# Optimization experiments

Hardware: AMD Instinct MI355X
Metric: run time of the kernel (lower is better)

## Reference

```python
import jax, jax.numpy as jnp
import numpy as np

B, L1, L2, D1, D2, H, P = 32, 256, 64, 256, 256, 256, 128
I = D1 + D2  # gate / GRU input dim


def setup_inputs() -> dict:
    key = jax.random.key(0)
    ks = jax.random.split(key, 10)
    s = 0.05  # weight init scale
    return {
        "sequence1": jax.random.normal(ks[0], (B, L1, D1), jnp.float32),
        "sequence2": jax.random.normal(ks[1], (B, L2, D2), jnp.float32),
        "sequence1_mask": jnp.ones((B, L1), jnp.float32),
        "sequence2_mask": jnp.ones((B, L2), jnp.float32),
        "W1": jax.random.normal(ks[2], (D2, P), jnp.float32) * s,
        "W2": jax.random.normal(ks[3], (D1 + H, P), jnp.float32) * s,
        "v": jax.random.normal(ks[4], (P,), jnp.float32) * s,
        "Wg": jax.random.normal(ks[5], (I, I), jnp.float32) * s,
        "bg": jnp.zeros((I,), jnp.float32),
        "w_ih": jax.random.normal(ks[6], (3 * H, I), jnp.float32) * s,
        "w_hh": jax.random.normal(ks[7], (3 * H, H), jnp.float32) * s,
        "b_ih": jnp.zeros((3 * H,), jnp.float32),
        "b_hh": jnp.zeros((3 * H,), jnp.float32),
    }


def reference(sequence1, sequence2, sequence1_mask, sequence2_mask,
              W1, W2, v, Wg, bg, w_ih, w_hh, b_ih, b_hh):
    # Precompute sequence2 projection once: [B, L2, P]
    seq2_proj = jnp.einsum('bld,dp->blp', sequence2, W1)
    # Additive mask for softmax over L2
    neg = jnp.where(sequence2_mask > 0, 0.0, -1e9)  # [B, L2]
    xs = jnp.transpose(sequence1, (1, 0, 2))  # [L1, B, D1]

    def step(h, x_t):
        # attention: v^T tanh(W1*seq2_j + W2*[x_t; h])
        vec = jnp.concatenate([x_t, h], axis=-1)            # [B, D1+H]
        s = jnp.einsum('blp,p->bl',
                       jnp.tanh(seq2_proj + (vec @ W2)[:, None, :]), v) + neg
        w = jax.nn.softmax(s, axis=-1)                      # [B, L2]
        att = jnp.einsum('bl,bld->bd', w, sequence2)        # [B, D2]
        inp = jnp.concatenate([x_t, att], axis=-1)          # [B, I]
        # gated attention: sigmoid(Linear(inp)) * inp
        inp = jax.nn.sigmoid(inp @ Wg.T + bg) * inp
        # GRUCell (torch semantics)
        gi = inp @ w_ih.T + b_ih
        gh = h @ w_hh.T + b_hh
        ir, iz, inn = jnp.split(gi, 3, axis=-1)
        hr, hz, hn = jnp.split(gh, 3, axis=-1)
        r = jax.nn.sigmoid(ir + hr)
        z = jax.nn.sigmoid(iz + hz)
        n = jnp.tanh(inn + r * hn)
        h_new = (1.0 - z) * n + z * h
        return h_new, h_new

    h0 = jnp.zeros((sequence1.shape[0], w_hh.shape[1]), sequence1.dtype)
    _, hs = jax.lax.scan(step, h0, xs)                      # [L1, B, H]
    out = jnp.transpose(hs, (1, 0, 2)) * sequence1_mask[:, :, None]
    return out
```

## Files before the change

### kernel.cpp

```cpp
#include <hip/hip_runtime.h>

typedef _Float16 half2_v __attribute__((ext_vector_type(2)));
typedef unsigned int u32;

#define W2K_O    0
#define WHHP_O   16384
#define WIHP_O   114688
#define NPACKW   311296
#define S2P_B    1245184
#define S2T_B    1769472
#define M1_B     2818048
#define PROJX_B  4915200
#define GATEX_B  7012352
#define EXCH_B   15400960

#define SMEM_BYTES 149520

__device__ __forceinline__ float fdot2(half2_v a, half2_v b, float c) {
    return __builtin_amdgcn_fdot2(a, b, c, false);
}
__device__ __forceinline__ half2_v h2_of(u32 u) { return __builtin_bit_cast(half2_v, u); }
__device__ __forceinline__ u32 pack_h2(float a, float b) {
    half2_v r; r[0] = (_Float16)a; r[1] = (_Float16)b;
    return __builtin_bit_cast(u32, r);
}
__device__ __forceinline__ float dot4(uint4 w, uint4 a, float acc) {
    acc = fdot2(h2_of(w.x), h2_of(a.x), acc);
    acc = fdot2(h2_of(w.y), h2_of(a.y), acc);
    acc = fdot2(h2_of(w.z), h2_of(a.z), acc);
    acc = fdot2(h2_of(w.w), h2_of(a.w), acc);
    return acc;
}
__device__ __forceinline__ float fast_tanh(float x) {
    float e = __expf(2.0f * x);
    return 1.0f - 2.0f / (e + 1.0f);
}
__device__ __forceinline__ float fast_sigmoid(float x) {
    return 1.0f / (1.0f + __expf(-x));
}
__device__ __forceinline__ u32 aload(const u32* p) {
    return __hip_atomic_load(p, __ATOMIC_RELAXED, __HIP_MEMORY_SCOPE_AGENT);
}
__device__ __forceinline__ void astore(u32* p, u32 v) {
    __hip_atomic_store(p, v, __ATOMIC_RELAXED, __HIP_MEMORY_SCOPE_AGENT);
}
__device__ __forceinline__ u32 mkw(float x, u32 st) {
    unsigned short hb = __builtin_bit_cast(unsigned short, (_Float16)x);
    return (st << 16) | (u32)hb;
}
__device__ __forceinline__ float f16low(u32 v) {
    return (float)__builtin_bit_cast(_Float16, (unsigned short)(v & 0xFFFFu));
}

__global__ void prep_pack_w(const float* __restrict__ W2, const float* __restrict__ wih,
                            const float* __restrict__ whh, u32* __restrict__ ws_u) {
    int idx = blockIdx.x * 256 + threadIdx.x;
    if (idx >= NPACKW) return;
    float a, c;
    if (idx < WHHP_O) {
        int mm = idx >> 11, r = idx & 2047, p = r >> 4, kl = r & 15;
        int row = 256 + mm * 32 + 2 * kl;
        a = W2[row * 128 + p]; c = W2[(row + 1) * 128 + p];
    } else if (idx < WIHP_O) {
        int t2 = idx - WHHP_O, mm = t2 / 12288, r = t2 % 12288, o = r >> 7, k = r & 127;
        int row = (o >> 5) * 256 + mm * 32 + (o & 31);
        a = whh[row * 256 + 2 * k]; c = whh[row * 256 + 2 * k + 1];
    } else {
        int t2 = idx - WIHP_O, mm = t2 / 24576, r = t2 % 24576, o = r >> 8, k = r & 255;
        int row = (o >> 5) * 256 + mm * 32 + (o & 31);
        a = wih[row * 512 + 2 * k]; c = wih[row * 512 + 2 * k + 1];
    }
    ws_u[idx] = pack_h2(a, c);
}

__global__ void prep_s2p(const float* __restrict__ seq2, const float* __restrict__ W1,
                         _Float16* __restrict__ outh) {
    int idx = blockIdx.x * 256 + threadIdx.x;
    int p = idx & 127, j = (idx >> 7) & 63, b = idx >> 13;
    const float* s2 = seq2 + (b * 64 + j) * 256;
    float acc = 0.f;
    #pragma unroll 8
    for (int d = 0; d < 256; ++d) acc += s2[d] * W1[d * 128 + p];
    outh[idx] = (_Float16)acc;
}

__global__ void prep_s2T(const float* __restrict__ seq2, _Float16* __restrict__ dst) {
    int idx = blockIdx.x * 256 + threadIdx.x;
    int j = idx & 63, d = (idx >> 6) & 255, b = idx >> 14;
    dst[idx] = (_Float16)seq2[(b * 64 + j) * 256 + d];
}

__global__ void prep_m1(const float* __restrict__ Wg, const float* __restrict__ seq2,
                        _Float16* __restrict__ dst) {
    int idx = blockIdx.x * 256 + threadIdx.x;
    int j = idx & 63, o = (idx >> 6) & 511, b = idx >> 15;
    const float* wr = Wg + o * 512 + 256;
    const float* s2 = seq2 + (b * 64 + j) * 256;
    float acc = 0.f;
    #pragma unroll 8
    for (int d = 0; d < 256; ++d) acc += wr[d] * s2[d];
    dst[idx] = (_Float16)acc;
}

__global__ void prep_gemm(const float* __restrict__ A, const float* __restrict__ Bsrc,
                          int mode, _Float16* __restrict__ C, int N) {
    __shared__ float As[64][17];
    __shared__ float Bs[16][65];
    int r0 = blockIdx.x * 64, n0 = blockIdx.y * 64;
    int tid = threadIdx.x;
    int tr = tid >> 4, tc = tid & 15;
    float acc[4][4] = {};
    for (int k0 = 0; k0 < 256; k0 += 16) {
        #pragma unroll
        for (int i = 0; i < 4; ++i) {
            int rr = (tid >> 4) + i * 16, kk = tid & 15;
            As[rr][kk] = A[(r0 + rr) * 256 + k0 + kk];
        }
        #pragma unroll
        for (int i = 0; i < 4; ++i) {
            if (mode == 0) { int kk = (tid >> 6) + i * 4, nn = tid & 63; Bs[kk][nn] = Bsrc[(k0 + kk) * N + n0 + nn]; }
            else           { int nn = (tid >> 4) + i * 16, kk = tid & 15; Bs[kk][nn] = Bsrc[(n0 + nn) * 512 + k0 + kk]; }
        }
        __syncthreads();
        #pragma unroll
        for (int k = 0; k < 16; ++k)
            #pragma unroll
            for (int i = 0; i < 4; ++i)
                #pragma unroll
                for (int j = 0; j < 4; ++j)
                    acc[i][j] += As[tr * 4 + i][k] * Bs[k][tc * 4 + j];
        __syncthreads();
    }
    for (int i = 0; i < 4; ++i)
        for (int j = 0; j < 4; ++j)
            C[(size_t)(r0 + tr * 4 + i) * N + n0 + tc * 4 + j] = (_Float16)acc[i][j];
}

__global__ void __launch_bounds__(1024) match_rnn(
    const float* __restrict__ seq1, const float* __restrict__ mask1,
    const float* __restrict__ mask2, const float* __restrict__ v,
    const float* __restrict__ bg, const float* __restrict__ bih,
    const float* __restrict__ bhh, char* __restrict__ ws, float* __restrict__ out)
{
    const int m = blockIdx.x >> 5;
    const int b = blockIdx.x & 31;
    const int tid = threadIdx.x;

    extern __shared__ char smem[];
    u32* s_whh4 = (u32*)smem;
    u32* s_wih4 = s_whh4 + 12288;
    u32* s_w2k  = s_wih4 + 12288;
    u32* s_s2pU = s_w2k + 2176;
    u32* s_m1u  = s_s2pU + 4608;
    u32* s_s2Tu = s_m1u + 2112;
    float* s_redA = (float*)(s_s2Tu + 2112);
    float* s_redD = s_redA + 96;
    u32* s_h2u  = (u32*)(s_redD + 96);
    u32* s_ip2a = s_h2u + 160;
    u32* s_ip2b = s_ip2a + 160;
    float* s_projh = (float*)(s_ip2b + 160);
    float* s_projx = s_projh + 144;
    float* s_v   = s_projx + 144;
    float* s_w   = s_v + 144;
    float* s_neg = s_w + 64;
    float* s_gx  = s_neg + 64;
    float* s_xc  = s_gx + 64;
    float* s_bg  = s_xc + 64;
    float* s_bih = s_bg + 64;
    float* s_bhh = s_bih + 96;
    float* s_hf  = s_bhh + 96;
    u32* s_hloc  = (u32*)(s_hf + 32);
    float* s_m1v = (float*)(s_hloc + 16);

    unsigned short* s_s2p  = (unsigned short*)s_s2pU;
    unsigned short* s_h2h  = (unsigned short*)s_h2u;
    unsigned short* s_ip2ah = (unsigned short*)s_ip2a;
    unsigned short* s_ip2bh = (unsigned short*)s_ip2b;

    const u32* wsrc = (const u32*)ws;

    for (int i = tid; i < 12288; i += 1024) {
        int o = i >> 7, k = i & 127, u = k >> 2;
        int du4 = ((o >> 3) * 256) + ((u & 3) * 64) + (((o & 7) << 3) | (u >> 2));
        s_whh4[du4 * 4 + (k & 3)] = wsrc[WHHP_O + m * 12288 + i];
    }
    for (int i = tid; i < 12288; i += 1024) {
        int o = i >> 7, k = i & 127, u = k >> 2;
        int du4 = ((o >> 3) * 256) + ((u & 3) * 64) + (((o & 7) << 3) | (u >> 2));
        s_wih4[du4 * 4 + (k & 3)] = wsrc[WIHP_O + m * 24576 + o * 256 + k];
    }
    for (int i = tid; i < 2048; i += 1024) {
        int p = i >> 4, kl = i & 15;
        s_w2k[p * 17 + kl] = wsrc[W2K_O + m * 2048 + i];
    }
    {
        const u32* s2src = wsrc + (S2P_B / 4) + b * 4096;
        for (int i = tid; i < 4096; i += 1024) {
            int j = i >> 6, kk = i & 63;
            s_s2pU[j * 72 + kk] = s2src[i];
        }
        const u32* m1src = wsrc + (M1_B / 4) + (b * 512 + m * 64) * 32;
        for (int i = tid; i < 2048; i += 1024) {
            int o = i >> 5, jw = i & 31;
            s_m1u[o * 33 + jw] = m1src[i];
        }
        if (m >= 4) {
            const u32* stsrc = wsrc + (S2T_B / 4) + (b * 256 + (m - 4) * 64) * 32;
            for (int i = tid; i < 2048; i += 1024) {
                int dd = i >> 5, jw = i & 31;
                s_s2Tu[dd * 33 + jw] = stsrc[i];
            }
        } else {
            for (int i = tid; i < 2112; i += 1024) s_s2Tu[i] = 0u;
        }
    }
    if (tid < 128) s_v[tid + (tid >> 3)] = v[tid];
    if (tid < 64) { s_neg[tid] = (mask2[b * 64 + tid] > 0.f) ? 0.f : -1e9f; s_bg[tid] = bg[m * 64 + tid]; }
    if (tid < 96) {
        int row = (tid >> 5) * 256 + m * 32 + (tid & 31);
        s_bih[tid] = bih[row]; s_bhh[tid] = bhh[row];
    }
    if (tid < 32) s_hf[tid] = 0.f;

    uint4 wiA = {}, wiB = {}, wiC = {}, wiD = {};
    const int oAD = ((tid >> 6) << 3) + ((tid & 63) >> 3);
    const int ksAD = tid & 7;
    if (tid < 768) {
        const uint4* wip = (const uint4*)(wsrc + WIHP_O + m * 24576 + oAD * 256 + 128 + ksAD * 16);
        wiA = wip[0]; wiB = wip[1]; wiC = wip[2]; wiD = wip[3];
    }

    u32* exch = (u32*)(ws + EXCH_B) + b * 2048;
    const u32* g_projx = (const u32*)(ws + PROJX_B);
    const u32* g_gatex = (const u32*)(ws + GATEX_B);

    int dead = 0;
    __syncthreads();

    for (int t = 0; t < 256; ++t) {
        const u32 st = (u32)(t + 1);
        float4 xv = {};
        u32 pxv = 0, gxv = 0; float mkv = 0.f;
        if (tid >= 896 && tid < 912) {
            if (m < 4)
                xv = ((const float4*)(seq1 + (size_t)(b * 256 + t) * 256 + m * 64))[tid - 896];
        } else if (tid >= 912 && tid < 976)
            pxv = g_projx[(b * 256 + t) * 64 + (tid - 912)];
        else if (tid >= 976 && tid < 1008)
            gxv = g_gatex[(b * 256 + t) * 256 + m * 32 + (tid - 976)];
        else if (tid == 1008)
            mkv = mask1[b * 256 + t];

        if (t > 0) {
            u32 v1, v2;
            const bool p2 = tid < 256;
            const u32 stp = (u32)t;
            if (!dead) {
                int sp = 0;
                for (;;) {
                    v1 = aload(exch + tid);
                    v2 = p2 ? aload(exch + 1024 + tid) : (stp << 16);
                    bool ok = ((v1 >> 16) == stp) && ((v2 >> 16) == stp);
                    if (__all((int)ok)) break;
                    __builtin_amdgcn_s_sleep(1);
                    if (++sp > (1 << 17)) { dead = 1; break; }
                }
            } else { v1 = aload(exch + tid); v2 = p2 ? aload(exch + 1024 + tid) : 0; }
            float ph = f16low(v1);
            ph += __shfl_down(ph, 4, 8);
            ph += __shfl_down(ph, 2, 8);
            ph += __shfl_down(ph, 1, 8);
            if ((tid & 7) == 0) { int p = tid >> 3; s_projh[p + (p >> 3)] = ph; }
            if (p2) {
                int k = tid;
                int pos = ((k >> 5) * 20 + ((k >> 1) & 15)) * 2 + (k & 1);
                s_h2h[pos] = (unsigned short)(v2 & 0xFFFFu);
            }
        } else {
            if (tid < 160) s_h2u[tid] = 0u;
            if (tid < 144) s_projh[tid] = 0.f;
        }
        if (tid >= 896 && tid < 912) {
            int q = tid - 896;
            s_xc[4 * q] = xv.x; s_xc[4 * q + 1] = xv.y; s_xc[4 * q + 2] = xv.z; s_xc[4 * q + 3] = xv.w;
        } else if (tid >= 912 && tid < 976) {
            half2_v h = h2_of(pxv); int i = tid - 912;
            int base = 2 * i + (i >> 2);
            s_projx[base] = (float)h[0]; s_projx[base + 1] = (float)h[1];
        } else if (tid >= 976 && tid < 1008) {
            half2_v h = h2_of(gxv); int i = tid - 976;
            s_gx[2 * i] = (float)h[0]; s_gx[2 * i + 1] = (float)h[1];
        } else if (tid == 1008) s_m1v[0] = mkv;
        __syncthreads();

        {
            int j = tid >> 4, pk = tid & 15, p0 = pk * 8, pb = pk * 9;
            uint4 sv = *(const uint4*)&s_s2p[j * 144 + p0];
            const u32* su = (const u32*)&sv;
            float acc = 0.f;
            #pragma unroll
            for (int q = 0; q < 4; ++q) {
                half2_v h = h2_of(su[q]);
                int pc = pb + 2 * q;
                float a0 = (float)h[0] + s_projx[pc] + s_projh[pc];
                float a1 = (float)h[1] + s_projx[pc + 1] + s_projh[pc + 1];
                acc += fast_tanh(a0) * s_v[pc];
                acc += fast_tanh(a1) * s_v[pc + 1];
            }
            acc += __shfl_down(acc, 8, 16);
            acc += __shfl_down(acc, 4, 16);
            acc += __shfl_down(acc, 2, 16);
            acc += __shfl_down(acc, 1, 16);
            if (pk == 0) s_w[j] = acc + s_neg[j];
        }
        __syncthreads();
        if (tid < 64) {
            float sc = s_w[tid], mx = sc;
            #pragma unroll
            for (int off = 32; off > 0; off >>= 1) mx = fmaxf(mx, __shfl_xor(mx, off));
            float e = __expf(sc - mx), s = e;
            #pragma unroll
            for (int off = 32; off > 0; off >>= 1) s += __shfl_xor(s, off);
            s_w[tid] = e / s;
        }
        __syncthreads();

        if (tid < 512) {
            int o = tid >> 3, r = tid & 7, q = r & 3;
            const u32* src = (r >= 4) ? &s_s2Tu[o * 33] : &s_m1u[o * 33];
            float acc = 0.f;
            #pragma unroll
            for (int c = 0; c < 8; ++c) {
                half2_v h = h2_of(src[q * 8 + c]);
                int j0 = (q * 8 + c) * 2;
                acc += (float)h[0] * s_w[j0] + (float)h[1] * s_w[j0 + 1];
            }
            acc += __shfl_down(acc, 2, 4);
            acc += __shfl_down(acc, 1, 4);
            float attv = __shfl_down(acc, 4, 8);
            if (r == 0) {
                float g = acc + s_gx[o] + s_bg[o];
                float inpv = (m < 4) ? s_xc[o] : attv;
                astore(&exch[1280 + m * 64 + o], mkw(fast_sigmoid(g) * inpv, st));
            }
        }
        if (tid < 768) {
            const uint4* wbase = (const uint4*)s_whh4 + (tid >> 6) * 256;
            float acc = 0.f;
            #pragma unroll
            for (int c = 0; c < 4; ++c) {
                uint4 wv4 = wbase[c * 64 + (tid & 63)];
                uint4 av = *(const uint4*)&s_h2u[ksAD * 20 + c * 4];
                acc = dot4(wv4, av, acc);
            }
            acc += __shfl_down(acc, 4, 8);
            acc += __shfl_down(acc, 2, 8);
            acc += __shfl_down(acc, 1, 8);
            if (ksAD == 0) s_redA[oAD] = acc + s_bhh[oAD];
        }
        if (tid < 512) {
            u32 vv;
            if (!dead) {
                int sp = 0;
                for (;;) {
                    vv = aload(exch + 1280 + tid);
                    if (__all((int)((vv >> 16) == st))) break;
                    __builtin_amdgcn_s_sleep(1);
                    if (++sp > (1 << 17)) { dead = 1; break; }
                }
            } else vv = aload(exch + 1280 + tid);
            int i = tid;
            if (i < 256) {
                int pos = ((i >> 5) * 20 + ((i >> 1) & 15)) * 2 + (i & 1);
                s_ip2ah[pos] = (unsigned short)(vv & 0xFFFFu);
            } else {
                int i2 = i - 256;
                int pos = ((i2 >> 5) * 20 + ((i2 >> 1) & 15)) * 2 + (i2 & 1);
                s_ip2bh[pos] = (unsigned short)(vv & 0xFFFFu);
            }
        }
        __syncthreads();

        if (tid < 768) {
            const uint4* wbase = (const uint4*)s_wih4 + (tid >> 6) * 256;
            float acc = 0.f;
            #pragma unroll
            for (int c = 0; c < 4; ++c) {
                uint4 wv4 = wbase[c * 64 + (tid & 63)];
                uint4 av = *(const uint4*)&s_ip2a[ksAD * 20 + c * 4];
                acc = dot4(wv4, av, acc);
            }
            acc = dot4(wiA, *(const uint4*)&s_ip2b[ksAD * 20 + 0],  acc);
            acc = dot4(wiB, *(const uint4*)&s_ip2b[ksAD * 20 + 4],  acc);
            acc = dot4(wiC, *(const uint4*)&s_ip2b[ksAD * 20 + 8],  acc);
            acc = dot4(wiD, *(const uint4*)&s_ip2b[ksAD * 20 + 12], acc);
            acc += __shfl_down(acc, 4, 8);
            acc += __shfl_down(acc, 2, 8);
            acc += __shfl_down(acc, 1, 8);
            if (ksAD == 0) s_redD[oAD] = acc + s_bih[oAD];
        }
        __syncthreads();

        if (tid < 32) {
            int o = tid;
            float r_ = fast_sigmoid(s_redD[o] + s_redA[o]);
            float z_ = fast_sigmoid(s_redD[32 + o] + s_redA[32 + o]);
            float n_ = fast_tanh(s_redD[64 + o] + r_ * s_redA[64 + o]);
            float hn = (1.f - z_) * n_ + z_ * s_hf[o];
            s_hf[o] = hn;
            out[(size_t)(b * 256 + t) * 256 + m * 32 + o] = hn * s_m1v[0];
            astore(&exch[1024 + m * 32 + o], mkw(hn, st));
            float nb = __shfl_down(hn, 1);
            if (!(o & 1)) s_hloc[o >> 1] = pack_h2(hn, nb);
        }
        __syncthreads();

        if (tid < 512) {
            int p = tid >> 2, kc = tid & 3;
            float a = 0.f;
            #pragma unroll
            for (int cc = 0; cc < 4; ++cc)
                a = fdot2(h2_of(s_w2k[p * 17 + kc * 4 + cc]), h2_of(s_hloc[kc * 4 + cc]), a);
            a += __shfl_down(a, 2, 4);
            a += __shfl_down(a, 1, 4);
            if (kc == 0) astore(&exch[p * 8 + m], mkw(a, st));
        }
    }
}

extern "C" void kernel_launch(void* const* d_in, const int* in_sizes, int n_in,
                              void* d_out, int out_size, void* d_ws, size_t ws_size,
                              hipStream_t stream) {
    const float* seq1  = (const float*)d_in[0];
    const float* seq2  = (const float*)d_in[1];
    const float* mask1 = (const float*)d_in[2];
    const float* mask2 = (const float*)d_in[3];
    const float* W1    = (const float*)d_in[4];
    const float* W2    = (const float*)d_in[5];
    const float* v     = (const float*)d_in[6];
    const float* Wg    = (const float*)d_in[7];
    const float* bg    = (const float*)d_in[8];
    const float* wih   = (const float*)d_in[9];
    const float* whh   = (const float*)d_in[10];
    const float* bih   = (const float*)d_in[11];
    const float* bhh   = (const float*)d_in[12];

    char* ws = (char*)d_ws;

    (void)hipFuncSetAttribute(reinterpret_cast<const void*>(match_rnn),
                              hipFuncAttributeMaxDynamicSharedMemorySize, SMEM_BYTES);

    prep_pack_w<<<dim3((NPACKW + 255) / 256), dim3(256), 0, stream>>>(W2, wih, whh, (u32*)ws);
    prep_s2p<<<dim3(1024), dim3(256), 0, stream>>>(seq2, W1, (_Float16*)(ws + S2P_B));
    prep_s2T<<<dim3(2048), dim3(256), 0, stream>>>(seq2, (_Float16*)(ws + S2T_B));
    prep_m1<<<dim3(4096), dim3(256), 0, stream>>>(Wg, seq2, (_Float16*)(ws + M1_B));
    prep_gemm<<<dim3(128, 2), dim3(256), 0, stream>>>(seq1, W2, 0, (_Float16*)(ws + PROJX_B), 128);
    prep_gemm<<<dim3(128, 8), dim3(256), 0, stream>>>(seq1, Wg, 1, (_Float16*)(ws + GATEX_B), 512);
    (void)hipMemsetAsync(ws + EXCH_B, 0, 262144, stream);
    match_rnn<<<dim3(256), dim3(1024), SMEM_BYTES, stream>>>(seq1, mask1, mask2, v, bg, bih, bhh, ws, (float*)d_out);
}
```

Measured before the change: 1.614 ms.

## Prefetch next-step inputs, spin before sleeping, pack softmax weights for fdot2

Loads of x_t, projx, gatex and the mask for step t+1 are issued after the first barrier of step t, so their global latency overlaps with the step's compute instead of sitting on the critical path. The cross-block spin-wait loops now poll a few times before calling s_sleep, which cuts wake-up latency when the exchange data arrives quickly. Softmax weights are packed into half2 and the attention weighted sum uses fdot2, halving the LDS reads and FLOPs in that loop. The cost is reduced precision for the attention weights and some extra register pressure.

```diff
diff --git a/kernel.cpp b/kernel.cpp
--- a/kernel.cpp
+++ b/kernel.cpp
@@ -14,7 +14,7 @@
 #define GATEX_B  7012352
 #define EXCH_B   15400960
 
-#define SMEM_BYTES 149520
+#define SMEM_BYTES 149648
 
 __device__ __forceinline__ float fdot2(half2_v a, half2_v b, float c) {
     return __builtin_amdgcn_fdot2(a, b, c, false);
@@ -162,7 +162,8 @@
     float* s_projx = s_projh + 144;
     float* s_v   = s_projx + 144;
     float* s_w   = s_v + 144;
-    float* s_neg = s_w + 64;
+    u32* s_wp   = (u32*)(s_w + 64);
+    float* s_neg = (float*)(s_wp + 32);
     float* s_gx  = s_neg + 64;
     float* s_xc  = s_gx + 64;
     float* s_bg  = s_xc + 64;
@@ -237,19 +238,20 @@
     int dead = 0;
     __syncthreads();
 
+    float4 xv = {};
+    u32 pxv = 0, gxv = 0; float mkv = 0.f;
+    if (tid >= 896 && tid < 912) {
+        if (m < 4)
+            xv = ((const float4*)(seq1 + (size_t)(b * 256 + 0) * 256 + m * 64))[tid - 896];
+    } else if (tid >= 912 && tid < 976)
+        pxv = g_projx[(b * 256 + 0) * 64 + (tid - 912)];
+    else if (tid >= 976 && tid < 1008)
+        gxv = g_gatex[(b * 256 + 0) * 256 + m * 32 + (tid - 976)];
+    else if (tid == 1008)
+        mkv = mask1[b * 256 + 0];
+
     for (int t = 0; t < 256; ++t) {
         const u32 st = (u32)(t + 1);
-        float4 xv = {};
-        u32 pxv = 0, gxv = 0; float mkv = 0.f;
-        if (tid >= 896 && tid < 912) {
-            if (m < 4)
-                xv = ((const float4*)(seq1 + (size_t)(b * 256 + t) * 256 + m * 64))[tid - 896];
-        } else if (tid >= 912 && tid < 976)
-            pxv = g_projx[(b * 256 + t) * 64 + (tid - 912)];
-        else if (tid >= 976 && tid < 1008)
-            gxv = g_gatex[(b * 256 + t) * 256 + m * 32 + (tid - 976)];
-        else if (tid == 1008)
-            mkv = mask1[b * 256 + t];
 
         if (t > 0) {
             u32 v1, v2;
@@ -262,8 +264,8 @@
                     v2 = p2 ? aload(exch + 1024 + tid) : (stp << 16);
                     bool ok = ((v1 >> 16) == stp) && ((v2 >> 16) == stp);
                     if (__all((int)ok)) break;
-                    __builtin_amdgcn_s_sleep(1);
-                    if (++sp > (1 << 17)) { dead = 1; break; }
+                    if (++sp > 4) __builtin_amdgcn_s_sleep(1);
+                    if (sp > (1 << 17)) { dead = 1; break; }
                 }
             } else { v1 = aload(exch + tid); v2 = p2 ? aload(exch + 1024 + tid) : 0; }
             float ph = f16low(v1);
@@ -293,6 +295,18 @@
         } else if (tid == 1008) s_m1v[0] = mkv;
         __syncthreads();
 
+        if (t + 1 < 256) {
+            if (tid >= 896 && tid < 912) {
+                if (m < 4)
+                    xv = ((const float4*)(seq1 + (size_t)(b * 256 + t + 1) * 256 + m * 64))[tid - 896];
+            } else if (tid >= 912 && tid < 976)
+                pxv = g_projx[(b * 256 + t + 1) * 64 + (tid - 912)];
+            else if (tid >= 976 && tid < 1008)
+                gxv = g_gatex[(b * 256 + t + 1) * 256 + m * 32 + (tid - 976)];
+            else if (tid == 1008)
+                mkv = mask1[b * 256 + t + 1];
+        }
+
         {
             int j = tid >> 4, pk = tid & 15, p0 = pk * 8, pb = pk * 9;
             uint4 sv = *(const uint4*)&s_s2p[j * 144 + p0];
@@ -321,7 +335,9 @@
             float e = __expf(sc - mx), s = e;
             #pragma unroll
             for (int off = 32; off > 0; off >>= 1) s += __shfl_xor(s, off);
-            s_w[tid] = e / s;
+            float wv = e / s;
+            float nb = __shfl_down(wv, 1);
+            if (!(tid & 1)) s_wp[tid >> 1] = pack_h2(wv, nb);
         }
         __syncthreads();
 
@@ -330,11 +346,8 @@
             const u32* src = (r >= 4) ? &s_s2Tu[o * 33] : &s_m1u[o * 33];
             float acc = 0.f;
             #pragma unroll
-            for (int c = 0; c < 8; ++c) {
-                half2_v h = h2_of(src[q * 8 + c]);
-                int j0 = (q * 8 + c) * 2;
-                acc += (float)h[0] * s_w[j0] + (float)h[1] * s_w[j0 + 1];
-            }
+            for (int c = 0; c < 8; ++c)
+                acc = fdot2(h2_of(src[q * 8 + c]), h2_of(s_wp[q * 8 + c]), acc);
             acc += __shfl_down(acc, 2, 4);
             acc += __shfl_down(acc, 1, 4);
             float attv = __shfl_down(acc, 4, 8);
@@ -365,8 +378,8 @@
                 for (;;) {
                     vv = aload(exch + 1280 + tid);
                     if (__all((int)((vv >> 16) == st))) break;
-                    __builtin_amdgcn_s_sleep(1);
-                    if (++sp > (1 << 17)) { dead = 1; break; }
+                    if (++sp > 4) __builtin_amdgcn_s_sleep(1);
+                    if (sp > (1 << 17)) { dead = 1; break; }
                 }
             } else vv = aload(exch + 1280 + tid);
             int i = tid;
```

Measured after the change: 1.729 ms. 1.07x slower.
